# Kernel tuning notes

Measured on AMD Instinct MI355X. Metric: run time of the kernel, lower is better.

Reference implementation:

```python
import jax, jax.numpy as jnp
import numpy as np

B, S, H, FF, E = 4, 4096, 1024, 4096, 8
EPS = 1e-5


def setup_inputs() -> dict:
    key = jax.random.key(0)
    ks = jax.random.split(key, 8)
    std = 0.02
    return {
        "x": jax.random.normal(ks[0], (B, S, H), jnp.float32),
        "norm_weight": jnp.ones((H,), jnp.float32),
        "router_w": jax.random.normal(ks[1], (E, H), jnp.float32) * std,
        "router_b": jnp.zeros((E,), jnp.float32),
        "fc1_w": jax.random.normal(ks[2], (E, FF, H), jnp.float32) * std,
        "fc1_b": jnp.zeros((E, FF), jnp.float32),
        "fc2_w": jax.random.normal(ks[3], (E, H, FF), jnp.float32) * std,
        "fc2_b": jnp.zeros((E, H), jnp.float32),
    }


def reference(x, norm_weight, router_w, router_b, fc1_w, fc1_b, fc2_w, fc2_b):
    b, s, h = x.shape
    T = b * s
    e = router_w.shape[0]
    cap = T // e  # expert capacity, capacity_factor = 1.0

    x_flat = x.reshape(T, h)
    # RMSNorm (pre-norm on MoE input)
    xn = x_flat * jax.lax.rsqrt(jnp.mean(x_flat * x_flat, axis=-1, keepdims=True) + EPS) * norm_weight

    # Router (no jitter: eval / jitter_noise=0)
    logits = xn @ router_w.T + router_b          # [T, E]
    probs = jax.nn.softmax(logits, axis=-1)       # [T, E]

    # Expert-choice routing: each expert picks its top-`cap` tokens by prob
    gates, idx = jax.lax.top_k(probs.T, cap)      # [E, cap], [E, cap]

    # Dispatch (gather) and grouped expert MLP
    xe = xn[idx]                                   # [E, cap, H]
    hmid = jnp.einsum('ech,efh->ecf', xe, fc1_w) + fc1_b[:, None, :]
    hmid = jax.nn.gelu(hmid, approximate=False)    # torch F.gelu default (exact)
    ye = jnp.einsum('ecf,ehf->ech', hmid, fc2_w) + fc2_b[:, None, :]

    # Combine: gated scatter-add back to token positions, normalize by gate sum
    flat_idx = idx.reshape(-1)                     # [E*cap]
    weighted = (ye * gates[..., None]).reshape(-1, h)
    out = jnp.zeros((T, h), x.dtype).at[flat_idx].add(weighted)
    gate_sums = jnp.zeros((T, 1), x.dtype).at[flat_idx].add(gates.reshape(-1, 1))
    out = out / jnp.maximum(gate_sums, 1e-9)       # unrouted tokens stay zero
    return out.reshape(b, s, h)
```

## Files before the change

### kernel.cpp

```cpp
#include <hip/hip_runtime.h>
#include <hip/hip_bf16.h>

#define T_TOK 16384
#define H_DIM 1024
#define FF_DIM 4096
#define NE 8
#define CAP 2048
#define EPS_F 1e-5f

#define BM2 256
#define BN2 256
#define BK2 32

typedef __attribute__((ext_vector_type(4))) float f32x4;
typedef __attribute__((ext_vector_type(8))) short bf16x8;
typedef unsigned long long u64;
typedef unsigned int u32;

__device__ inline void gload_lds16(const void* g, void* l) {
  __builtin_amdgcn_global_load_lds(
      (const __attribute__((address_space(1))) unsigned int*)g,
      (__attribute__((address_space(3))) unsigned int*)l, 16, 0, 0);
}

__device__ inline unsigned short bf16_bits(float f) {
  __hip_bfloat16 h = __float2bfloat16(f);
  unsigned short u;
  __builtin_memcpy(&u, &h, 2);
  return u;
}

__device__ inline float bits_f32(unsigned short u) {
  const u32 x = ((u32)u) << 16;
  float f;
  __builtin_memcpy(&f, &x, 4);
  return f;
}

__global__ __launch_bounds__(256) void router_kernel(
    const float* __restrict__ x, const float* __restrict__ nw,
    const float* __restrict__ rw, const float* __restrict__ rb,
    __hip_bfloat16* __restrict__ xn, u64* __restrict__ keys) {
  const int t = blockIdx.x;
  const int tid = threadIdx.x;
  const float4 v = reinterpret_cast<const float4*>(x + (size_t)t * H_DIM)[tid];
  float ss = v.x * v.x + v.y * v.y + v.z * v.z + v.w * v.w;
#pragma unroll
  for (int o = 32; o > 0; o >>= 1) ss += __shfl_down(ss, o);
  __shared__ float red[4];
  __shared__ float redl[4][NE];
  const int wv = tid >> 6, ln = tid & 63;
  if (ln == 0) red[wv] = ss;
  __syncthreads();
  const float tot = red[0] + red[1] + red[2] + red[3];
  const float scale = rsqrtf(tot * (1.0f / H_DIM) + EPS_F);
  const float4 w4 = reinterpret_cast<const float4*>(nw)[tid];
  float xv0 = v.x * scale * w4.x, xv1 = v.y * scale * w4.y;
  float xv2 = v.z * scale * w4.z, xv3 = v.w * scale * w4.w;
  ushort4 u4;
  u4.x = bf16_bits(xv0); u4.y = bf16_bits(xv1);
  u4.z = bf16_bits(xv2); u4.w = bf16_bits(xv3);
  reinterpret_cast<ushort4*>(xn + (size_t)t * H_DIM)[tid] = u4;
  float lg[NE];
#pragma unroll
  for (int e = 0; e < NE; ++e) {
    const float4 r4 = reinterpret_cast<const float4*>(rw + (size_t)e * H_DIM)[tid];
    lg[e] = xv0 * r4.x + xv1 * r4.y + xv2 * r4.z + xv3 * r4.w;
  }
#pragma unroll
  for (int o = 32; o > 0; o >>= 1) {
#pragma unroll
    for (int e = 0; e < NE; ++e) lg[e] += __shfl_down(lg[e], o);
  }
  if (ln == 0) {
#pragma unroll
    for (int e = 0; e < NE; ++e) redl[wv][e] = lg[e];
  }
  __syncthreads();
  if (tid == 0) {
    float l[NE];
    float m = -1e30f;
#pragma unroll
    for (int e = 0; e < NE; ++e) {
      l[e] = redl[0][e] + redl[1][e] + redl[2][e] + redl[3][e] + rb[e];
      m = fmaxf(m, l[e]);
    }
    float s = 0.f;
#pragma unroll
    for (int e = 0; e < NE; ++e) { l[e] = expf(l[e] - m); s += l[e]; }
    const float inv = 1.0f / s;
#pragma unroll
    for (int e = 0; e < NE; ++e) {
      const float p = l[e] * inv;
      const u64 key = ((u64)__float_as_uint(p) << 32) | (u32)(0xFFFFFFFFu - (u32)t);
      keys[(size_t)e * T_TOK + t] = key;
    }
  }
}

__global__ __launch_bounds__(1024) void topk_kernel(
    const u64* __restrict__ keys, int* __restrict__ idxl,
    float* __restrict__ gatel, int* __restrict__ tok_list, int* __restrict__ tok_cnt) {
  const int e = blockIdx.x;
  const int tid = threadIdx.x;
  const int lane = tid & 63;
  const u64* ke = keys + (size_t)e * T_TOK;
  __shared__ int hist[256];
  __shared__ u64 s_pref;
  __shared__ int s_k;
  __shared__ int s_cnt;
  u64 pref = 0;
  int pbits = 0;
  int kneed = CAP;
  for (int pass = 0; pass < 8; ++pass) {
    if (tid < 256) hist[tid] = 0;
    __syncthreads();
    const int shift = 56 - 8 * pass;
    for (int i = tid; i < T_TOK; i += 1024) {
      const u64 key = ke[i];
      const bool ok = (pbits == 0) || ((key >> (64 - pbits)) == pref);
      const int d = ok ? (int)((key >> shift) & 255) : -1;
      u64 act = __ballot(ok);
      while (act) {
        const int src = __ffsll((long long)act) - 1;
        const int dl = __shfl(d, src);
        const u64 mb = __ballot(ok && (d == dl));
        if (lane == src) atomicAdd(&hist[dl], (int)__popcll(mb));
        act &= ~mb;
      }
    }
    __syncthreads();
    if (tid == 0) {
      int cum = 0;
      int d = 255;
      for (; d >= 0; --d) {
        cum += hist[d];
        if (cum >= kneed) break;
      }
      s_k = kneed - (cum - hist[d]);
      s_pref = (pref << 8) | (u64)(u32)d;
    }
    __syncthreads();
    pref = s_pref;
    kneed = s_k;
    pbits += 8;
    __syncthreads();
  }
  if (tid == 0) s_cnt = 0;
  __syncthreads();
  for (int i = tid; i < T_TOK; i += 1024) {
    const u64 key = ke[i];
    if (key >= pref) {
      const int pos = atomicAdd(&s_cnt, 1);
      if (pos < CAP) {
        const int tok = (int)(0xFFFFFFFFu - (u32)(key & 0xFFFFFFFFu));
        const float p = __uint_as_float((u32)(key >> 32));
        idxl[e * CAP + pos] = tok;
        gatel[e * CAP + pos] = p;
        const int j = atomicAdd(tok_cnt + tok, 1);
        if (j < NE) tok_list[tok * NE + j] = e * CAP + pos;
      }
    }
  }
}

__global__ __launch_bounds__(256) void cvt2_kernel(
    const float* __restrict__ s1, __hip_bfloat16* __restrict__ d1,
    const float* __restrict__ s2, __hip_bfloat16* __restrict__ d2, int n4each) {
  int i = blockIdx.x * blockDim.x + threadIdx.x;
  const int stride = gridDim.x * blockDim.x;
  for (; i < 2 * n4each; i += stride) {
    const float* s = (i < n4each) ? s1 : s2;
    __hip_bfloat16* d = (i < n4each) ? d1 : d2;
    const int j = (i < n4each) ? i : i - n4each;
    const float4 v = reinterpret_cast<const float4*>(s)[j];
    ushort4 o;
    o.x = bf16_bits(v.x); o.y = bf16_bits(v.y);
    o.z = bf16_bits(v.z); o.w = bf16_bits(v.w);
    reinterpret_cast<ushort4*>(d)[j] = o;
  }
}

template <int MODE>
__global__ __launch_bounds__(512, 2) void gemm4_kernel(
    const __hip_bfloat16* __restrict__ Asrc, const __hip_bfloat16* __restrict__ Bw,
    const float* __restrict__ bias, const int* __restrict__ idxl,
    const float* __restrict__ gatel, __hip_bfloat16* __restrict__ hmid,
    __hip_bfloat16* __restrict__ ye, int ebase) {
  constexpr int N = (MODE == 0) ? FF_DIM : H_DIM;
  constexpr int K = (MODE == 0) ? H_DIM : FF_DIM;
  constexpr int NBN = N / BN2;
  constexpr int LOG_NBN = (MODE == 0) ? 4 : 2;
  constexpr int BPE = (CAP / BM2) * NBN;
  constexpr int LOG_BPE = (MODE == 0) ? 7 : 5;
  constexpr int NT = K / BK2;

  const int nwg = gridDim.x;
  const int wg0 = blockIdx.x;
  const int wg = (wg0 & 7) * (nwg >> 3) + (wg0 >> 3);
  const int z = wg >> LOG_BPE;
  const int rr = wg & (BPE - 1);
  const int bm = rr >> LOG_NBN;
  const int bn = rr & (NBN - 1);
  const int e = ebase + z;

  const int tid = threadIdx.x;
  const int lane = tid & 63;
  const int w = tid >> 6;
  const int wr = w >> 2, wc = w & 3;
  const int fr = lane & 15, q = lane >> 4;

  __shared__ char smem[131072];

  const int srow = tid >> 2;
  const int sg = tid & 3;
  const int skoff = (sg ^ ((srow >> 1) & 3)) * 8;

  const __hip_bfloat16* asrc0;
  const __hip_bfloat16* asrc1;
  if constexpr (MODE == 0) {
    const int t0 = idxl[e * CAP + bm * BM2 + srow];
    const int t1 = idxl[e * CAP + bm * BM2 + 128 + srow];
    asrc0 = Asrc + (size_t)t0 * H_DIM + skoff;
    asrc1 = Asrc + (size_t)t1 * H_DIM + skoff;
  } else {
    asrc0 = Asrc + ((size_t)z * CAP + bm * BM2 + srow) * FF_DIM + skoff;
    asrc1 = asrc0 + (size_t)128 * FF_DIM;
  }
  const __hip_bfloat16* bsrc0 = Bw + (size_t)z * N * K + (size_t)(bn * BN2 + srow) * K + skoff;
  const __hip_bfloat16* bsrc1 = bsrc0 + (size_t)128 * K;

  const int slot = ((q ^ ((fr >> 1) & 3)) << 4);
  int offA[8], offB[4];
#pragma unroll
  for (int m = 0; m < 8; ++m) offA[m] = (wr * 128 + m * 16 + fr) * 64 + slot;
#pragma unroll
  for (int n = 0; n < 4; ++n) offB[n] = 16384 + (wc * 64 + n * 16 + fr) * 64 + slot;

  f32x4 acc[8][4] = {};

#define STAGE4(buf, kt)                                     \
  do {                                                      \
    const int k0_ = (kt)*BK2;                               \
    char* d_ = smem + (buf)*32768 + tid * 16;               \
    gload_lds16(asrc0 + k0_, d_);                           \
    gload_lds16(asrc1 + k0_, d_ + 8192);                    \
    gload_lds16(bsrc0 + k0_, d_ + 16384);                   \
    gload_lds16(bsrc1 + k0_, d_ + 24576);                   \
  } while (0)

  STAGE4(0, 0);
  STAGE4(1, 1);
  STAGE4(2, 2);

  for (int kt = 0; kt < NT; ++kt) {
    const int cur = kt & 3;
    const int pf = (kt + 3 < NT) ? (kt + 3) : (kt + 3 - NT);
    const int k0p = pf * BK2;
    char* pdst = smem + ((kt + 3) & 3) * 32768 + tid * 16;

    asm volatile("s_waitcnt vmcnt(8)");
    __builtin_amdgcn_s_barrier();
    __builtin_amdgcn_sched_barrier(0);

    const char* base = smem + cur * 32768;
    bf16x8 af[8], bfr[4];
#pragma unroll
    for (int n = 0; n < 4; ++n) bfr[n] = *reinterpret_cast<const bf16x8*>(base + offB[n]);
#pragma unroll
    for (int m = 0; m < 8; ++m) af[m] = *reinterpret_cast<const bf16x8*>(base + offA[m]);
    gload_lds16(asrc0 + k0p, pdst);
    gload_lds16(asrc1 + k0p, pdst + 8192);
    gload_lds16(bsrc0 + k0p, pdst + 16384);
    gload_lds16(bsrc1 + k0p, pdst + 24576);
    __builtin_amdgcn_sched_barrier(0);

    __builtin_amdgcn_s_setprio(1);
#pragma unroll
    for (int m = 0; m < 8; ++m) {
#pragma unroll
      for (int n = 0; n < 4; ++n)
        acc[m][n] = __builtin_amdgcn_mfma_f32_16x16x32_bf16(af[m], bfr[n], acc[m][n], 0, 0, 0);
    }
    __builtin_amdgcn_s_setprio(0);
  }
#undef STAGE4

  if constexpr (MODE == 0) {
#pragma unroll
    for (int m = 0; m < 8; ++m) {
      const int rbase = bm * BM2 + wr * 128 + m * 16 + q * 4;
#pragma unroll
      for (int n = 0; n < 4; ++n) {
        const int gn = bn * BN2 + wc * 64 + n * 16 + fr;
        const float bb = bias[e * FF_DIM + gn];
#pragma unroll
        for (int i = 0; i < 4; ++i) {
          const float v = acc[m][n][i] + bb;
          const float u = v * (1.5957691216f + 0.0713548162972f * v * v);
          const float s = 1.0f / (1.0f + __expf(-u));
          hmid[((size_t)z * CAP + rbase + i) * FF_DIM + gn] = __float2bfloat16(v * s);
        }
      }
    }
  } else {
#pragma unroll
    for (int m = 0; m < 8; ++m) {
      const int rbase = bm * BM2 + wr * 128 + m * 16 + q * 4;
      float gt[4];
#pragma unroll
      for (int i = 0; i < 4; ++i) gt[i] = gatel[e * CAP + rbase + i];
#pragma unroll
      for (int n = 0; n < 4; ++n) {
        const int gn = bn * BN2 + wc * 64 + n * 16 + fr;
        const float bb = bias[e * H_DIM + gn];
#pragma unroll
        for (int i = 0; i < 4; ++i)
          ye[((size_t)e * CAP + rbase + i) * H_DIM + gn] =
              __float2bfloat16((acc[m][n][i] + bb) * gt[i]);
      }
    }
  }
}

__global__ __launch_bounds__(256) void combine_kernel(
    const __hip_bfloat16* __restrict__ ye, const float* __restrict__ gatel,
    const int* __restrict__ tok_list, const int* __restrict__ tok_cnt,
    float* __restrict__ out) {
  const int t = blockIdx.x;
  const int tid = threadIdx.x;
  const int cnt = tok_cnt[t];
  float a0 = 0.f, a1 = 0.f, a2 = 0.f, a3 = 0.f, gs = 0.f;
  for (int j = 0; j < cnt && j < NE; ++j) {
    const int ent = tok_list[t * NE + j];
    gs += gatel[ent];
    const ushort4 v = reinterpret_cast<const ushort4*>(ye + (size_t)ent * H_DIM)[tid];
    a0 += bits_f32(v.x);
    a1 += bits_f32(v.y);
    a2 += bits_f32(v.z);
    a3 += bits_f32(v.w);
  }
  const float inv = 1.0f / fmaxf(gs, 1e-9f);
  float4 o;
  o.x = a0 * inv; o.y = a1 * inv; o.z = a2 * inv; o.w = a3 * inv;
  reinterpret_cast<float4*>(out + (size_t)t * H_DIM)[tid] = o;
}

extern "C" void kernel_launch(void* const* d_in, const int* in_sizes, int n_in,
                              void* d_out, int out_size, void* d_ws, size_t ws_size,
                              hipStream_t stream) {
  const float* x = (const float*)d_in[0];
  const float* nw = (const float*)d_in[1];
  const float* rw = (const float*)d_in[2];
  const float* rb = (const float*)d_in[3];
  const float* fc1w = (const float*)d_in[4];
  const float* fc1b = (const float*)d_in[5];
  const float* fc2w = (const float*)d_in[6];
  const float* fc2b = (const float*)d_in[7];
  float* out = (float*)d_out;

  char* ws = (char*)d_ws;
  size_t off = 0;
  auto alloc = [&](size_t b) {
    char* p = ws + off;
    off += (b + 255) & ~(size_t)255;
    return p;
  };
  __hip_bfloat16* xn = (__hip_bfloat16*)alloc((size_t)T_TOK * H_DIM * 2);
  u64* keys = (u64*)alloc((size_t)NE * T_TOK * 8);
  int* idxl = (int*)alloc((size_t)NE * CAP * 4);
  float* gatel = (float*)alloc((size_t)NE * CAP * 4);
  int* tok_list = (int*)alloc((size_t)T_TOK * NE * 4);
  int* tok_cnt = (int*)alloc((size_t)T_TOK * 4);
  __hip_bfloat16* ye = (__hip_bfloat16*)alloc((size_t)NE * CAP * H_DIM * 2);

  int EC = NE;
  while (EC > 1) {
    const size_t per = (size_t)EC * ((size_t)FF_DIM * H_DIM * 2 * 2 + (size_t)CAP * FF_DIM * 2);
    if (off + per + 4096 <= ws_size) break;
    EC >>= 1;
  }
  __hip_bfloat16* w1b = (__hip_bfloat16*)alloc((size_t)EC * FF_DIM * H_DIM * 2);
  __hip_bfloat16* w2b = (__hip_bfloat16*)alloc((size_t)EC * H_DIM * FF_DIM * 2);
  __hip_bfloat16* hmid = (__hip_bfloat16*)alloc((size_t)EC * CAP * FF_DIM * 2);

  hipMemsetAsync(tok_cnt, 0, (size_t)T_TOK * 4, stream);

  router_kernel<<<T_TOK, 256, 0, stream>>>(x, nw, rw, rb, xn, keys);
  topk_kernel<<<NE, 1024, 0, stream>>>(keys, idxl, gatel, tok_list, tok_cnt);

  for (int eb = 0; eb < NE; eb += EC) {
    const int n4 = EC * FF_DIM * H_DIM / 4;
    cvt2_kernel<<<4096, 256, 0, stream>>>(fc1w + (size_t)eb * FF_DIM * H_DIM, w1b,
                                          fc2w + (size_t)eb * H_DIM * FF_DIM, w2b, n4);
    const int nb1 = EC * (CAP / BM2) * (FF_DIM / BN2);
    gemm4_kernel<0><<<nb1, 512, 0, stream>>>(xn, w1b, fc1b, idxl, gatel, hmid, ye, eb);
    const int nb2 = EC * (CAP / BM2) * (H_DIM / BN2);
    gemm4_kernel<1><<<nb2, 512, 0, stream>>>(hmid, w2b, fc2b, idxl, gatel, hmid, ye, eb);
  }
  combine_kernel<<<T_TOK, 256, 0, stream>>>(ye, gatel, tok_list, tok_cnt, out);
}
```

Baseline: 567.9 us.

## Split GEMM k-step into four quadrant phases interleaving LDS reads, loads and MFMAs

The main GEMM loop now splits each k-tile into four 4x2 MFMA quadrants. It interleaves LDS fragment reads and global-to-LDS prefetch loads between the quadrants, with barriers and priority changes around each block. The aim is to overlap LDS read latency and global load issue with MFMA execution and to lower live fragment registers. In exchange it adds more barriers per iteration and needs a careful vmcnt ordering to stay correct.

```diff
diff --git a/kernel.cpp b/kernel.cpp
--- a/kernel.cpp
+++ b/kernel.cpp
@@ -182,7 +182,7 @@
 }
 
 template <int MODE>
-__global__ __launch_bounds__(512, 2) void gemm4_kernel(
+__global__ __launch_bounds__(512, 2) void gemm5_kernel(
     const __hip_bfloat16* __restrict__ Asrc, const __hip_bfloat16* __restrict__ Bw,
     const float* __restrict__ bias, const int* __restrict__ idxl,
     const float* __restrict__ gatel, __hip_bfloat16* __restrict__ hmid,
@@ -230,61 +230,95 @@
   const __hip_bfloat16* bsrc0 = Bw + (size_t)z * N * K + (size_t)(bn * BN2 + srow) * K + skoff;
   const __hip_bfloat16* bsrc1 = bsrc0 + (size_t)128 * K;
 
-  const int slot = ((q ^ ((fr >> 1) & 3)) << 4);
-  int offA[8], offB[4];
-#pragma unroll
-  for (int m = 0; m < 8; ++m) offA[m] = (wr * 128 + m * 16 + fr) * 64 + slot;
-#pragma unroll
-  for (int n = 0; n < 4; ++n) offB[n] = 16384 + (wc * 64 + n * 16 + fr) * 64 + slot;
+  const int slotk = ((q ^ ((fr >> 1) & 3)) << 4);
+  int aoff[4], boff[2];
+#pragma unroll
+  for (int m = 0; m < 4; ++m) aoff[m] = (wr * 128 + m * 16 + fr) * 64 + slotk;
+#pragma unroll
+  for (int n = 0; n < 2; ++n) boff[n] = 16384 + (wc * 64 + n * 16 + fr) * 64 + slotk;
 
   f32x4 acc[8][4] = {};
-
-#define STAGE4(buf, kt)                                     \
-  do {                                                      \
-    const int k0_ = (kt)*BK2;                               \
-    char* d_ = smem + (buf)*32768 + tid * 16;               \
-    gload_lds16(asrc0 + k0_, d_);                           \
-    gload_lds16(asrc1 + k0_, d_ + 8192);                    \
-    gload_lds16(bsrc0 + k0_, d_ + 16384);                   \
-    gload_lds16(bsrc1 + k0_, d_ + 24576);                   \
+  bf16x8 Aa[4], Ab[4], Bb0[2], Bb1[2];
+
+#define GLD(sb, part, src, k0) \
+  gload_lds16((src) + (k0), smem + (sb)*32768 + (part)*8192 + tid * 16)
+
+#define RD_A(dst, sb, mh)                                          \
+  do {                                                             \
+    const char* b_ = smem + (sb)*32768 + (mh)*4096;                \
+    dst[0] = *reinterpret_cast<const bf16x8*>(b_ + aoff[0]);       \
+    dst[1] = *reinterpret_cast<const bf16x8*>(b_ + aoff[1]);       \
+    dst[2] = *reinterpret_cast<const bf16x8*>(b_ + aoff[2]);       \
+    dst[3] = *reinterpret_cast<const bf16x8*>(b_ + aoff[3]);       \
   } while (0)
 
-  STAGE4(0, 0);
-  STAGE4(1, 1);
-  STAGE4(2, 2);
+#define RD_B(dst, sb, nh)                                          \
+  do {                                                             \
+    const char* b_ = smem + (sb)*32768 + (nh)*2048;                \
+    dst[0] = *reinterpret_cast<const bf16x8*>(b_ + boff[0]);       \
+    dst[1] = *reinterpret_cast<const bf16x8*>(b_ + boff[1]);       \
+  } while (0)
+
+#define MM8(Af, Bf, mh, nh)                                                        \
+  do {                                                                             \
+    _Pragma("unroll") for (int m_ = 0; m_ < 4; ++m_) {                             \
+      _Pragma("unroll") for (int n_ = 0; n_ < 2; ++n_) {                           \
+        acc[(mh)*4 + m_][(nh)*2 + n_] = __builtin_amdgcn_mfma_f32_16x16x32_bf16(   \
+            Af[m_], Bf[n_], acc[(mh)*4 + m_][(nh)*2 + n_], 0, 0, 0);               \
+      }                                                                            \
+    }                                                                              \
+  } while (0)
+
+  GLD(0, 0, asrc0, 0); GLD(0, 1, asrc1, 0); GLD(0, 2, bsrc0, 0); GLD(0, 3, bsrc1, 0);
+  GLD(1, 0, asrc0, BK2); GLD(1, 1, asrc1, BK2); GLD(1, 2, bsrc0, BK2); GLD(1, 3, bsrc1, BK2);
+  GLD(2, 0, asrc0, 2 * BK2); GLD(2, 1, asrc1, 2 * BK2); GLD(2, 2, bsrc0, 2 * BK2); GLD(2, 3, bsrc1, 2 * BK2);
+  asm volatile("s_waitcnt vmcnt(8)");
+  __builtin_amdgcn_s_barrier();
+  RD_A(Aa, 0, 0);
+  RD_B(Bb0, 0, 0);
 
   for (int kt = 0; kt < NT; ++kt) {
-    const int cur = kt & 3;
-    const int pf = (kt + 3 < NT) ? (kt + 3) : (kt + 3 - NT);
-    const int k0p = pf * BK2;
-    char* pdst = smem + ((kt + 3) & 3) * 32768 + tid * 16;
-
-    asm volatile("s_waitcnt vmcnt(8)");
+    const int scur = kt & 3, snxt = (kt + 1) & 3, psl = (kt + 3) & 3;
+    const int kref = (kt + 3 < NT) ? (kt + 3) : (kt + 3 - NT);
+    const int k0p = kref * BK2;
+    RD_B(Bb1, scur, 1);
+    GLD(psl, 0, asrc0, k0p);
     __builtin_amdgcn_s_barrier();
     __builtin_amdgcn_sched_barrier(0);
-
-    const char* base = smem + cur * 32768;
-    bf16x8 af[8], bfr[4];
-#pragma unroll
-    for (int n = 0; n < 4; ++n) bfr[n] = *reinterpret_cast<const bf16x8*>(base + offB[n]);
-#pragma unroll
-    for (int m = 0; m < 8; ++m) af[m] = *reinterpret_cast<const bf16x8*>(base + offA[m]);
-    gload_lds16(asrc0 + k0p, pdst);
-    gload_lds16(asrc1 + k0p, pdst + 8192);
-    gload_lds16(bsrc0 + k0p, pdst + 16384);
-    gload_lds16(bsrc1 + k0p, pdst + 24576);
+    __builtin_amdgcn_s_setprio(1);
+    MM8(Aa, Bb0, 0, 0);
+    __builtin_amdgcn_s_setprio(0);
+    __builtin_amdgcn_s_barrier();
+    RD_A(Ab, scur, 1);
+    GLD(psl, 1, asrc1, k0p);
+    __builtin_amdgcn_s_barrier();
     __builtin_amdgcn_sched_barrier(0);
-
     __builtin_amdgcn_s_setprio(1);
-#pragma unroll
-    for (int m = 0; m < 8; ++m) {
-#pragma unroll
-      for (int n = 0; n < 4; ++n)
-        acc[m][n] = __builtin_amdgcn_mfma_f32_16x16x32_bf16(af[m], bfr[n], acc[m][n], 0, 0, 0);
-    }
+    MM8(Aa, Bb1, 0, 1);
     __builtin_amdgcn_s_setprio(0);
-  }
-#undef STAGE4
+    __builtin_amdgcn_s_barrier();
+    GLD(psl, 2, bsrc0, k0p);
+    asm volatile("s_waitcnt vmcnt(7)");
+    __builtin_amdgcn_s_barrier();
+    __builtin_amdgcn_sched_barrier(0);
+    __builtin_amdgcn_s_setprio(1);
+    MM8(Ab, Bb0, 1, 0);
+    __builtin_amdgcn_s_setprio(0);
+    __builtin_amdgcn_s_barrier();
+    RD_A(Aa, snxt, 0);
+    RD_B(Bb0, snxt, 0);
+    GLD(psl, 3, bsrc1, k0p);
+    __builtin_amdgcn_s_barrier();
+    __builtin_amdgcn_sched_barrier(0);
+    __builtin_amdgcn_s_setprio(1);
+    MM8(Ab, Bb1, 1, 1);
+    __builtin_amdgcn_s_setprio(0);
+    __builtin_amdgcn_s_barrier();
+  }
+#undef GLD
+#undef RD_A
+#undef RD_B
+#undef MM8
 
   if constexpr (MODE == 0) {
 #pragma unroll
@@ -394,9 +428,9 @@
     cvt2_kernel<<<4096, 256, 0, stream>>>(fc1w + (size_t)eb * FF_DIM * H_DIM, w1b,
                                           fc2w + (size_t)eb * H_DIM * FF_DIM, w2b, n4);
     const int nb1 = EC * (CAP / BM2) * (FF_DIM / BN2);
-    gemm4_kernel<0><<<nb1, 512, 0, stream>>>(xn, w1b, fc1b, idxl, gatel, hmid, ye, eb);
+    gemm5_kernel<0><<<nb1, 512, 0, stream>>>(xn, w1b, fc1b, idxl, gatel, hmid, ye, eb);
     const int nb2 = EC * (CAP / BM2) * (H_DIM / BN2);
-    gemm4_kernel<1><<<nb2, 512, 0, stream>>>(hmid, w2b, fc2b, idxl, gatel, hmid, ye, eb);
+    gemm5_kernel<1><<<nb2, 512, 0, stream>>>(hmid, w2b, fc2b, idxl, gatel, hmid, ye, eb);
   }
   combine_kernel<<<T_TOK, 256, 0, stream>>>(ye, gatel, tok_list, tok_cnt, out);
 }
```

After: 555.5 us. 1.02x faster.

## Split GEMM main loop into two half-phases interleaving loads, barriers and MFMAs

Applied to the files above, without the earlier changes.

Restructures the K-loop of the grouped expert GEMM into two phases. The first phase computes with the first half of the A fragments while the A-tile prefetch is issued. The second phase issues the B-tile prefetch, then computes with the second half of the A fragments. LDS reads and global-to-LDS loads are spread across two barriers per iteration, with finer vmcnt/lgkmcnt waits, to overlap memory traffic with MFMA work. This adds a second workgroup barrier per iteration, and the correctness of the buffer-reuse ordering depends on the hand-tuned wait counts.

```diff
diff --git a/kernel.cpp b/kernel.cpp
--- a/kernel.cpp
+++ b/kernel.cpp
@@ -182,7 +182,7 @@
 }
 
 template <int MODE>
-__global__ __launch_bounds__(512, 2) void gemm4_kernel(
+__global__ __launch_bounds__(512, 2) void gemm6_kernel(
     const __hip_bfloat16* __restrict__ Asrc, const __hip_bfloat16* __restrict__ Bw,
     const float* __restrict__ bias, const int* __restrict__ idxl,
     const float* __restrict__ gatel, __hip_bfloat16* __restrict__ hmid,
@@ -230,61 +230,90 @@
   const __hip_bfloat16* bsrc0 = Bw + (size_t)z * N * K + (size_t)(bn * BN2 + srow) * K + skoff;
   const __hip_bfloat16* bsrc1 = bsrc0 + (size_t)128 * K;
 
-  const int slot = ((q ^ ((fr >> 1) & 3)) << 4);
-  int offA[8], offB[4];
-#pragma unroll
-  for (int m = 0; m < 8; ++m) offA[m] = (wr * 128 + m * 16 + fr) * 64 + slot;
-#pragma unroll
-  for (int n = 0; n < 4; ++n) offB[n] = 16384 + (wc * 64 + n * 16 + fr) * 64 + slot;
+  const int slotk = ((q ^ ((fr >> 1) & 3)) << 4);
+  int aoff[8], boff[4];
+#pragma unroll
+  for (int m = 0; m < 8; ++m) aoff[m] = (wr * 128 + m * 16 + fr) * 64 + slotk;
+#pragma unroll
+  for (int n = 0; n < 4; ++n) boff[n] = 16384 + (wc * 64 + n * 16 + fr) * 64 + slotk;
 
   f32x4 acc[8][4] = {};
-
-#define STAGE4(buf, kt)                                     \
-  do {                                                      \
-    const int k0_ = (kt)*BK2;                               \
-    char* d_ = smem + (buf)*32768 + tid * 16;               \
-    gload_lds16(asrc0 + k0_, d_);                           \
-    gload_lds16(asrc1 + k0_, d_ + 8192);                    \
-    gload_lds16(bsrc0 + k0_, d_ + 16384);                   \
-    gload_lds16(bsrc1 + k0_, d_ + 24576);                   \
+  bf16x8 Aa[4], Ab[4], B0f[2], B1f[2];
+
+#define GLDA(sb, k0)                                             \
+  do {                                                           \
+    char* d_ = smem + (sb)*32768 + tid * 16;                     \
+    gload_lds16(asrc0 + (k0), d_);                               \
+    gload_lds16(asrc1 + (k0), d_ + 8192);                        \
   } while (0)
-
-  STAGE4(0, 0);
-  STAGE4(1, 1);
-  STAGE4(2, 2);
+#define GLDB(sb, k0)                                             \
+  do {                                                           \
+    char* d_ = smem + (sb)*32768 + tid * 16;                     \
+    gload_lds16(bsrc0 + (k0), d_ + 16384);                       \
+    gload_lds16(bsrc1 + (k0), d_ + 24576);                       \
+  } while (0)
+
+  GLDA(0, 0); GLDB(0, 0);
+  GLDA(1, BK2); GLDB(1, BK2);
+  GLDA(2, 2 * BK2); GLDB(2, 2 * BK2);
+  asm volatile("s_waitcnt vmcnt(4)");
+  __builtin_amdgcn_s_barrier();
+  __builtin_amdgcn_sched_barrier(0);
 
   for (int kt = 0; kt < NT; ++kt) {
     const int cur = kt & 3;
-    const int pf = (kt + 3 < NT) ? (kt + 3) : (kt + 3 - NT);
-    const int k0p = pf * BK2;
-    char* pdst = smem + ((kt + 3) & 3) * 32768 + tid * 16;
-
-    asm volatile("s_waitcnt vmcnt(8)");
+    const int kref = (kt + 3 < NT) ? (kt + 3) : (kt + 3 - NT);
+    const int k0p = kref * BK2;
+    const int psl = (kt + 3) & 3;
+    const char* base = smem + cur * 32768;
+
+    Aa[0] = *reinterpret_cast<const bf16x8*>(base + aoff[0]);
+    Aa[1] = *reinterpret_cast<const bf16x8*>(base + aoff[1]);
+    Aa[2] = *reinterpret_cast<const bf16x8*>(base + aoff[2]);
+    Aa[3] = *reinterpret_cast<const bf16x8*>(base + aoff[3]);
+    B0f[0] = *reinterpret_cast<const bf16x8*>(base + boff[0]);
+    B0f[1] = *reinterpret_cast<const bf16x8*>(base + boff[1]);
+    B1f[0] = *reinterpret_cast<const bf16x8*>(base + boff[2]);
+    B1f[1] = *reinterpret_cast<const bf16x8*>(base + boff[3]);
+    __builtin_amdgcn_sched_barrier(0);
+    Ab[0] = *reinterpret_cast<const bf16x8*>(base + aoff[4]);
+    Ab[1] = *reinterpret_cast<const bf16x8*>(base + aoff[5]);
+    Ab[2] = *reinterpret_cast<const bf16x8*>(base + aoff[6]);
+    Ab[3] = *reinterpret_cast<const bf16x8*>(base + aoff[7]);
+    GLDA(psl, k0p);
+    asm volatile("s_waitcnt vmcnt(6)");
     __builtin_amdgcn_s_barrier();
-    __builtin_amdgcn_sched_barrier(0);
-
-    const char* base = smem + cur * 32768;
-    bf16x8 af[8], bfr[4];
-#pragma unroll
-    for (int n = 0; n < 4; ++n) bfr[n] = *reinterpret_cast<const bf16x8*>(base + offB[n]);
-#pragma unroll
-    for (int m = 0; m < 8; ++m) af[m] = *reinterpret_cast<const bf16x8*>(base + offA[m]);
-    gload_lds16(asrc0 + k0p, pdst);
-    gload_lds16(asrc1 + k0p, pdst + 8192);
-    gload_lds16(bsrc0 + k0p, pdst + 16384);
-    gload_lds16(bsrc1 + k0p, pdst + 24576);
-    __builtin_amdgcn_sched_barrier(0);
-
+    asm volatile("s_waitcnt lgkmcnt(4)");
+    __builtin_amdgcn_sched_barrier(0);
     __builtin_amdgcn_s_setprio(1);
 #pragma unroll
-    for (int m = 0; m < 8; ++m) {
-#pragma unroll
-      for (int n = 0; n < 4; ++n)
-        acc[m][n] = __builtin_amdgcn_mfma_f32_16x16x32_bf16(af[m], bfr[n], acc[m][n], 0, 0, 0);
+    for (int m_ = 0; m_ < 4; ++m_) {
+      acc[m_][0] = __builtin_amdgcn_mfma_f32_16x16x32_bf16(Aa[m_], B0f[0], acc[m_][0], 0, 0, 0);
+      acc[m_][1] = __builtin_amdgcn_mfma_f32_16x16x32_bf16(Aa[m_], B0f[1], acc[m_][1], 0, 0, 0);
+      acc[m_][2] = __builtin_amdgcn_mfma_f32_16x16x32_bf16(Aa[m_], B1f[0], acc[m_][2], 0, 0, 0);
+      acc[m_][3] = __builtin_amdgcn_mfma_f32_16x16x32_bf16(Aa[m_], B1f[1], acc[m_][3], 0, 0, 0);
     }
     __builtin_amdgcn_s_setprio(0);
-  }
-#undef STAGE4
+    __builtin_amdgcn_sched_barrier(0);
+
+    GLDB(psl, k0p);
+    asm volatile("s_waitcnt lgkmcnt(0)");
+    __builtin_amdgcn_sched_barrier(0);
+    __builtin_amdgcn_s_barrier();
+    __builtin_amdgcn_sched_barrier(0);
+    __builtin_amdgcn_s_setprio(1);
+#pragma unroll
+    for (int m_ = 0; m_ < 4; ++m_) {
+      acc[4 + m_][0] = __builtin_amdgcn_mfma_f32_16x16x32_bf16(Ab[m_], B0f[0], acc[4 + m_][0], 0, 0, 0);
+      acc[4 + m_][1] = __builtin_amdgcn_mfma_f32_16x16x32_bf16(Ab[m_], B0f[1], acc[4 + m_][1], 0, 0, 0);
+      acc[4 + m_][2] = __builtin_amdgcn_mfma_f32_16x16x32_bf16(Ab[m_], B1f[0], acc[4 + m_][2], 0, 0, 0);
+      acc[4 + m_][3] = __builtin_amdgcn_mfma_f32_16x16x32_bf16(Ab[m_], B1f[1], acc[4 + m_][3], 0, 0, 0);
+    }
+    __builtin_amdgcn_s_setprio(0);
+    __builtin_amdgcn_sched_barrier(0);
+  }
+#undef GLDA
+#undef GLDB
 
   if constexpr (MODE == 0) {
 #pragma unroll
@@ -394,9 +423,9 @@
     cvt2_kernel<<<4096, 256, 0, stream>>>(fc1w + (size_t)eb * FF_DIM * H_DIM, w1b,
                                           fc2w + (size_t)eb * H_DIM * FF_DIM, w2b, n4);
     const int nb1 = EC * (CAP / BM2) * (FF_DIM / BN2);
-    gemm4_kernel<0><<<nb1, 512, 0, stream>>>(xn, w1b, fc1b, idxl, gatel, hmid, ye, eb);
+    gemm6_kernel<0><<<nb1, 512, 0, stream>>>(xn, w1b, fc1b, idxl, gatel, hmid, ye, eb);
     const int nb2 = EC * (CAP / BM2) * (H_DIM / BN2);
-    gemm4_kernel<1><<<nb2, 512, 0, stream>>>(hmid, w2b, fc2b, idxl, gatel, hmid, ye, eb);
+    gemm6_kernel<1><<<nb2, 512, 0, stream>>>(hmid, w2b, fc2b, idxl, gatel, hmid, ye, eb);
   }
   combine_kernel<<<T_TOK, 256, 0, stream>>>(ye, gatel, tok_list, tok_cnt, out);
 }
```

New measurement: 547.8 us. 1.04x faster.

## Restructure expert GEMM to 16 waves with BK=64 double buffering; faster top-k

Applied to the files above, without the earlier changes.

The expert GEMMs now run 1024-thread workgroups (16 waves, each owning a 64x64 sub-tile) with a K-tile of 64 and two 64KB LDS buffers, replacing the 4-stage BK=32 ring with 8 waves. A new XOR swizzle over 8 chunks matches the wider rows. The aim is more waves to hide latency and fewer barriers per K. The cost is a full vmcnt(0) wait at every step, which weakens overlap. Top-k now radix-selects on only the upper 32 bits, then resolves ties from a small LDS list, removing four of the eight full passes over the keys.

```diff
diff --git a/kernel.cpp b/kernel.cpp
--- a/kernel.cpp
+++ b/kernel.cpp
@@ -10,7 +10,7 @@
 
 #define BM2 256
 #define BN2 256
-#define BK2 32
+#define BK64 64
 
 typedef __attribute__((ext_vector_type(4))) float f32x4;
 typedef __attribute__((ext_vector_type(8))) short bf16x8;
@@ -98,6 +98,7 @@
   }
 }
 
+#define EQCAP 7168
 __global__ __launch_bounds__(1024) void topk_kernel(
     const u64* __restrict__ keys, int* __restrict__ idxl,
     float* __restrict__ gatel, int* __restrict__ tok_list, int* __restrict__ tok_cnt) {
@@ -106,20 +107,23 @@
   const int lane = tid & 63;
   const u64* ke = keys + (size_t)e * T_TOK;
   __shared__ int hist[256];
-  __shared__ u64 s_pref;
+  __shared__ u32 s_pref;
   __shared__ int s_k;
   __shared__ int s_cnt;
-  u64 pref = 0;
+  __shared__ int s_eq;
+  __shared__ u32 eqlist[EQCAP];
+
+  u32 pref = 0;
   int pbits = 0;
   int kneed = CAP;
-  for (int pass = 0; pass < 8; ++pass) {
+  for (int pass = 0; pass < 4; ++pass) {
     if (tid < 256) hist[tid] = 0;
     __syncthreads();
-    const int shift = 56 - 8 * pass;
+    const int shift = 24 - 8 * pass;
     for (int i = tid; i < T_TOK; i += 1024) {
-      const u64 key = ke[i];
-      const bool ok = (pbits == 0) || ((key >> (64 - pbits)) == pref);
-      const int d = ok ? (int)((key >> shift) & 255) : -1;
+      const u32 hi = (u32)(ke[i] >> 32);
+      const bool ok = (pbits == 0) || ((hi >> (32 - pbits)) == pref);
+      const int d = ok ? (int)((hi >> shift) & 255) : -1;
       u64 act = __ballot(ok);
       while (act) {
         const int src = __ffsll((long long)act) - 1;
@@ -138,7 +142,7 @@
         if (cum >= kneed) break;
       }
       s_k = kneed - (cum - hist[d]);
-      s_pref = (pref << 8) | (u64)(u32)d;
+      s_pref = (pref << 8) | (u32)d;
     }
     __syncthreads();
     pref = s_pref;
@@ -146,19 +150,114 @@
     pbits += 8;
     __syncthreads();
   }
-  if (tid == 0) s_cnt = 0;
+  const u32 thrp = pref;
+  const float thrp_f = __uint_as_float(thrp);
+
+  if (tid == 0) { s_cnt = 0; s_eq = 0; }
   __syncthreads();
   for (int i = tid; i < T_TOK; i += 1024) {
     const u64 key = ke[i];
-    if (key >= pref) {
+    const u32 hi = (u32)(key >> 32);
+    if (hi > thrp) {
       const int pos = atomicAdd(&s_cnt, 1);
       if (pos < CAP) {
-        const int tok = (int)(0xFFFFFFFFu - (u32)(key & 0xFFFFFFFFu));
-        const float p = __uint_as_float((u32)(key >> 32));
+        const int tok = (int)(0xFFFFFFFFu - (u32)key);
         idxl[e * CAP + pos] = tok;
-        gatel[e * CAP + pos] = p;
+        gatel[e * CAP + pos] = __uint_as_float(hi);
         const int j = atomicAdd(tok_cnt + tok, 1);
         if (j < NE) tok_list[tok * NE + j] = e * CAP + pos;
+      }
+    } else if (hi == thrp) {
+      const int j = atomicAdd(&s_eq, 1);
+      if (j < EQCAP) eqlist[j] = (u32)key;
+    }
+  }
+  __syncthreads();
+  const int neq = s_eq;
+  if (neq <= EQCAP) {
+    u32 prefl = 0;
+    int pb = 0;
+    int kn = kneed;
+    if (neq > kneed) {
+      for (int pass = 0; pass < 4; ++pass) {
+        if (tid < 256) hist[tid] = 0;
+        __syncthreads();
+        const int shift = 24 - 8 * pass;
+        for (int i = tid; i < neq; i += 1024) {
+          const u32 vv = eqlist[i];
+          if ((pb == 0) || ((vv >> (32 - pb)) == prefl)) atomicAdd(&hist[(vv >> shift) & 255], 1);
+        }
+        __syncthreads();
+        if (tid == 0) {
+          int cum = 0;
+          int d = 255;
+          for (; d >= 0; --d) {
+            cum += hist[d];
+            if (cum >= kn) break;
+          }
+          s_k = kn - (cum - hist[d]);
+          s_pref = (prefl << 8) | (u32)d;
+        }
+        __syncthreads();
+        prefl = s_pref;
+        kn = s_k;
+        pb += 8;
+        __syncthreads();
+      }
+    }
+    for (int i = tid; i < neq; i += 1024) {
+      const u32 lo = eqlist[i];
+      if (neq <= kneed || lo >= prefl) {
+        const int pos = atomicAdd(&s_cnt, 1);
+        if (pos < CAP) {
+          const int tok = (int)(0xFFFFFFFFu - lo);
+          idxl[e * CAP + pos] = tok;
+          gatel[e * CAP + pos] = thrp_f;
+          const int j = atomicAdd(tok_cnt + tok, 1);
+          if (j < NE) tok_list[tok * NE + j] = e * CAP + pos;
+        }
+      }
+    }
+  } else {
+    u64 pref64 = (u64)thrp;
+    int pb64 = 32;
+    int kn = kneed;
+    for (int pass = 4; pass < 8; ++pass) {
+      if (tid < 256) hist[tid] = 0;
+      __syncthreads();
+      const int shift = 56 - 8 * pass;
+      for (int i = tid; i < T_TOK; i += 1024) {
+        const u64 key = ke[i];
+        if ((key >> (64 - pb64)) == pref64) atomicAdd(&hist[(int)((key >> shift) & 255)], 1);
+      }
+      __syncthreads();
+      if (tid == 0) {
+        int cum = 0;
+        int d = 255;
+        for (; d >= 0; --d) {
+          cum += hist[d];
+          if (cum >= kn) break;
+        }
+        s_k = kn - (cum - hist[d]);
+        s_pref = (u32)d;
+      }
+      __syncthreads();
+      pref64 = (pref64 << 8) | s_pref;
+      kn = s_k;
+      pb64 += 8;
+      __syncthreads();
+    }
+    for (int i = tid; i < T_TOK; i += 1024) {
+      const u64 key = ke[i];
+      if ((u32)(key >> 32) == thrp && key >= pref64) {
+        const int pos = atomicAdd(&s_cnt, 1);
+        if (pos < CAP) {
+          const int tok = (int)(0xFFFFFFFFu - (u32)key);
+          idxl[e * CAP + pos] = tok;
+          gatel[e * CAP + pos] = thrp_f;
+          const int j = atomicAdd(tok_cnt + tok, 1);
+          if (j < NE) tok_list[tok * NE + j] = e * CAP + pos;
+        }
       }
     }
   }
@@ -182,7 +281,7 @@
 }
 
 template <int MODE>
-__global__ __launch_bounds__(512, 2) void gemm4_kernel(
+__global__ __launch_bounds__(1024, 4) void gemm8_kernel(
     const __hip_bfloat16* __restrict__ Asrc, const __hip_bfloat16* __restrict__ Bw,
     const float* __restrict__ bias, const int* __restrict__ idxl,
     const float* __restrict__ gatel, __hip_bfloat16* __restrict__ hmid,
@@ -193,7 +292,7 @@
   constexpr int LOG_NBN = (MODE == 0) ? 4 : 2;
   constexpr int BPE = (CAP / BM2) * NBN;
   constexpr int LOG_BPE = (MODE == 0) ? 7 : 5;
-  constexpr int NT = K / BK2;
+  constexpr int NT = K / BK64;
 
   const int nwg = gridDim.x;
   const int wg0 = blockIdx.x;
@@ -212,9 +311,9 @@
 
   __shared__ char smem[131072];
 
-  const int srow = tid >> 2;
-  const int sg = tid & 3;
-  const int skoff = (sg ^ ((srow >> 1) & 3)) * 8;
+  const int srow = tid >> 3;
+  const int sg = tid & 7;
+  const int skoff = (sg ^ (srow & 7)) * 8;
 
   const __hip_bfloat16* asrc0;
   const __hip_bfloat16* asrc1;
@@ -230,66 +329,86 @@
   const __hip_bfloat16* bsrc0 = Bw + (size_t)z * N * K + (size_t)(bn * BN2 + srow) * K + skoff;
   const __hip_bfloat16* bsrc1 = bsrc0 + (size_t)128 * K;
 
-  const int slot = ((q ^ ((fr >> 1) & 3)) << 4);
-  int offA[8], offB[4];
-#pragma unroll
-  for (int m = 0; m < 8; ++m) offA[m] = (wr * 128 + m * 16 + fr) * 64 + slot;
-#pragma unroll
-  for (int n = 0; n < 4; ++n) offB[n] = 16384 + (wc * 64 + n * 16 + fr) * 64 + slot;
-
-  f32x4 acc[8][4] = {};
-
-#define STAGE4(buf, kt)                                     \
-  do {                                                      \
-    const int k0_ = (kt)*BK2;                               \
-    char* d_ = smem + (buf)*32768 + tid * 16;               \
-    gload_lds16(asrc0 + k0_, d_);                           \
-    gload_lds16(asrc1 + k0_, d_ + 8192);                    \
-    gload_lds16(bsrc0 + k0_, d_ + 16384);                   \
-    gload_lds16(bsrc1 + k0_, d_ + 24576);                   \
+  int aoffs[4][2], boffs[4][2];
+#pragma unroll
+  for (int m = 0; m < 4; ++m) {
+    const int row = wr * 64 + m * 16 + fr;
+#pragma unroll
+    for (int ks = 0; ks < 2; ++ks)
+      aoffs[m][ks] = row * 128 + (((ks * 4 + q) ^ (row & 7)) << 4);
+  }
+#pragma unroll
+  for (int n = 0; n < 4; ++n) {
+    const int row = wc * 64 + n * 16 + fr;
+#pragma unroll
+    for (int ks = 0; ks < 2; ++ks)
+      boffs[n][ks] = 32768 + row * 128 + (((ks * 4 + q) ^ (row & 7)) << 4);
+  }
+
+  f32x4 acc[4][4] = {};
+  bf16x8 Af[4], Bf[4];
+
+#define STAGE8(sb, k0)                                       \
+  do {                                                       \
+    char* d_ = smem + (sb)*65536 + tid * 16;                 \
+    gload_lds16(asrc0 + (k0), d_);                           \
+    gload_lds16(asrc1 + (k0), d_ + 16384);                   \
+    gload_lds16(bsrc0 + (k0), d_ + 32768);                   \
+    gload_lds16(bsrc1 + (k0), d_ + 49152);                   \
   } while (0)
 
-  STAGE4(0, 0);
-  STAGE4(1, 1);
-  STAGE4(2, 2);
+  STAGE8(0, 0);
+  asm volatile("s_waitcnt vmcnt(0)");
+  __builtin_amdgcn_s_barrier();
+  __builtin_amdgcn_sched_barrier(0);
 
   for (int kt = 0; kt < NT; ++kt) {
-    const int cur = kt & 3;
-    const int pf = (kt + 3 < NT) ? (kt + 3) : (kt + 3 - NT);
-    const int k0p = pf * BK2;
-    char* pdst = smem + ((kt + 3) & 3) * 32768 + tid * 16;
-
-    asm volatile("s_waitcnt vmcnt(8)");
+    const char* base = smem + (kt & 1) * 65536;
+    if (kt + 1 < NT) STAGE8((kt + 1) & 1, (kt + 1) * BK64);
+    Af[0] = *reinterpret_cast<const bf16x8*>(base + aoffs[0][0]);
+    Af[1] = *reinterpret_cast<const bf16x8*>(base + aoffs[1][0]);
+    Af[2] = *reinterpret_cast<const bf16x8*>(base + aoffs[2][0]);
+    Af[3] = *reinterpret_cast<const bf16x8*>(base + aoffs[3][0]);
+    Bf[0] = *reinterpret_cast<const bf16x8*>(base + boffs[0][0]);
+    Bf[1] = *reinterpret_cast<const bf16x8*>(base + boffs[1][0]);
+    Bf[2] = *reinterpret_cast<const bf16x8*>(base + boffs[2][0]);
+    Bf[3] = *reinterpret_cast<const bf16x8*>(base + boffs[3][0]);
+    asm volatile("s_waitcnt lgkmcnt(0)");
+    __builtin_amdgcn_sched_barrier(0);
+    __builtin_amdgcn_s_setprio(1);
+#pragma unroll
+    for (int m_ = 0; m_ < 4; ++m_)
+#pragma unroll
+      for (int n_ = 0; n_ < 4; ++n_)
+        acc[m_][n_] = __builtin_amdgcn_mfma_f32_16x16x32_bf16(Af[m_], Bf[n_], acc[m_][n_], 0, 0, 0);
+    __builtin_amdgcn_s_setprio(0);
+    Af[0] = *reinterpret_cast<const bf16x8*>(base + aoffs[0][1]);
+    Af[1] = *reinterpret_cast<const bf16x8*>(base + aoffs[1][1]);
+    Af[2] = *reinterpret_cast<const bf16x8*>(base + aoffs[2][1]);
+    Af[3] = *reinterpret_cast<const bf16x8*>(base + aoffs[3][1]);
+    Bf[0] = *reinterpret_cast<const bf16x8*>(base + boffs[0][1]);
+    Bf[1] = *reinterpret_cast<const bf16x8*>(base + boffs[1][1]);
+    Bf[2] = *reinterpret_cast<const bf16x8*>(base + boffs[2][1]);
+    Bf[3] = *reinterpret_cast<const bf16x8*>(base + boffs[3][1]);
+    asm volatile("s_waitcnt lgkmcnt(0)");
+    __builtin_amdgcn_sched_barrier(0);
+    __builtin_amdgcn_s_setprio(1);
+#pragma unroll
+    for (int m_ = 0; m_ < 4; ++m_)
+#pragma unroll
+      for (int n_ = 0; n_ < 4; ++n_)
+        acc[m_][n_] = __builtin_amdgcn_mfma_f32_16x16x32_bf16(Af[m_], Bf[n_], acc[m_][n_], 0, 0, 0);
+    __builtin_amdgcn_s_setprio(0);
+    asm volatile("s_waitcnt vmcnt(0)");
     __builtin_amdgcn_s_barrier();
     __builtin_amdgcn_sched_barrier(0);
-
-    const char* base = smem + cur * 32768;
-    bf16x8 af[8], bfr[4];
-#pragma unroll
-    for (int n = 0; n < 4; ++n) bfr[n] = *reinterpret_cast<const bf16x8*>(base + offB[n]);
-#pragma unroll
-    for (int m = 0; m < 8; ++m) af[m] = *reinterpret_cast<const bf16x8*>(base + offA[m]);
-    gload_lds16(asrc0 + k0p, pdst);
-    gload_lds16(asrc1 + k0p, pdst + 8192);
-    gload_lds16(bsrc0 + k0p, pdst + 16384);
-    gload_lds16(bsrc1 + k0p, pdst + 24576);
-    __builtin_amdgcn_sched_barrier(0);
-
-    __builtin_amdgcn_s_setprio(1);
-#pragma unroll
-    for (int m = 0; m < 8; ++m) {
-#pragma unroll
-      for (int n = 0; n < 4; ++n)
-        acc[m][n] = __builtin_amdgcn_mfma_f32_16x16x32_bf16(af[m], bfr[n], acc[m][n], 0, 0, 0);
-    }
-    __builtin_amdgcn_s_setprio(0);
-  }
-#undef STAGE4
+  }
+#undef STAGE8
 
   if constexpr (MODE == 0) {
 #pragma unroll
-    for (int m = 0; m < 8; ++m) {
-      const int rbase = bm * BM2 + wr * 128 + m * 16 + q * 4;
+    for (int m = 0; m < 4; ++m) {
+      const int rbase = bm * BM2 + wr * 64 + m * 16 + q * 4;
 #pragma unroll
       for (int n = 0; n < 4; ++n) {
         const int gn = bn * BN2 + wc * 64 + n * 16 + fr;
@@ -305,8 +424,8 @@
     }
   } else {
 #pragma unroll
-    for (int m = 0; m < 8; ++m) {
-      const int rbase = bm * BM2 + wr * 128 + m * 16 + q * 4;
+    for (int m = 0; m < 4; ++m) {
+      const int rbase = bm * BM2 + wr * 64 + m * 16 + q * 4;
       float gt[4];
 #pragma unroll
       for (int i = 0; i < 4; ++i) gt[i] = gatel[e * CAP + rbase + i];
@@ -394,9 +513,9 @@
     cvt2_kernel<<<4096, 256, 0, stream>>>(fc1w + (size_t)eb * FF_DIM * H_DIM, w1b,
                                           fc2w + (size_t)eb * H_DIM * FF_DIM, w2b, n4);
     const int nb1 = EC * (CAP / BM2) * (FF_DIM / BN2);
-    gemm4_kernel<0><<<nb1, 512, 0, stream>>>(xn, w1b, fc1b, idxl, gatel, hmid, ye, eb);
+    gemm8_kernel<0><<<nb1, 1024, 0, stream>>>(xn, w1b, fc1b, idxl, gatel, hmid, ye, eb);
     const int nb2 = EC * (CAP / BM2) * (H_DIM / BN2);
-    gemm4_kernel<1><<<nb2, 512, 0, stream>>>(hmid, w2b, fc2b, idxl, gatel, hmid, ye, eb);
+    gemm8_kernel<1><<<nb2, 1024, 0, stream>>>(hmid, w2b, fc2b, idxl, gatel, hmid, ye, eb);
   }
   combine_kernel<<<T_TOK, 256, 0, stream>>>(ye, gatel, tok_list, tok_cnt, out);
 }
```

Result: faster. 533.7 us (-6.0%).
